# Optimization experiments

Hardware: AMD Instinct MI355X
Metric: run time of the kernel (lower is better)

Reference implementation:

```python
import jax, jax.numpy as jnp
import numpy as np

NX = NY = 2048
DT = 0.01
DX = 1.0
DY = 1.0
RE = 1.0
NLEVEL = int(np.log2(NY)) + 1  # 12 levels


def pad_zero(x):
    # Dirichlet (zero) halo of width 1: matches boundary_condition_u/v/k/cw
    return jnp.pad(x, ((0, 0), (0, 0), (1, 1), (1, 1)))


def pad_edge(x):
    # Edge-replicate halo (incl. corners): matches boundary_condition_p
    return jnp.pad(x, ((0, 0), (0, 0), (1, 1), (1, 1)), mode='edge')


def conv2d(x, w, stride=1):
    return jax.lax.conv_general_dilated(
        x, w, (stride, stride), 'VALID',
        dimension_numbers=('NCHW', 'OIHW', 'NCHW'))


def upsample2(x):
    return jnp.repeat(jnp.repeat(x, 2, axis=2), 2, axis=3)


def pg_vector(u, v, pad_u, pad_v, k1, ADx_u, ADy_u, ADx_v, ADy_v, AD2_u, AD2_v, w_diff):
    # Petrov-Galerkin dissipation. pad_u/pad_v are the padded ORIGINAL velocities:
    # the torch code references the global values_uu/values_vv buffers here.
    k_u = 0.25 * DX * jnp.abs(0.5 * DX ** -3 * (jnp.abs(u) * DX + jnp.abs(v) * DY) * AD2_u) \
        / (0.001 + (jnp.abs(ADx_u) * DX ** -3 + jnp.abs(ADy_u) * DX ** -3) / 2.0)
    k_v = 0.25 * DY * jnp.abs(0.5 * DX ** -3 * (jnp.abs(u) * DX + jnp.abs(v) * DY) * AD2_v) \
        / (0.001 + (jnp.abs(ADx_v) * DX ** -3 + jnp.abs(ADy_v) * DX ** -3) / 2.0)
    k_u = jnp.minimum(k_u, k1)
    k_v = jnp.minimum(k_v, k1)
    k_uu = pad_zero(k_u)
    k_vv = pad_zero(k_v)
    k_x = 1.5 * (k_u * AD2_u + conv2d(pad_u * k_uu, w_diff) - u * conv2d(k_uu, w_diff))
    k_y = 1.5 * (k_v * AD2_v + conv2d(pad_v * k_vv, w_diff) - v * conv2d(k_vv, w_diff))
    return k_x, k_y


def f_cycle_mg(pad_u, pad_v, values_p, iteration, w_A, w_res, w_xadv, w_yadv):
    diag = w_A[0, 0, 1, 1]
    b = -(conv2d(pad_u, w_xadv) + conv2d(pad_v, w_yadv)) / DT
    w = jnp.zeros((1, 1, 2, 2), values_p.dtype)
    r = b
    for _ in range(iteration):
        w = jnp.zeros((1, 1, 2, 2), values_p.dtype)
        r = conv2d(pad_edge(values_p), w_A) - b
        r_s = [r]
        for _i in range(1, NLEVEL - 1):
            r = conv2d(r, w_res, stride=2)  # restriction down to 2x2
            r_s.append(r)
        for i in reversed(range(1, NLEVEL - 1)):
            w = w - conv2d(pad_zero(w), w_A) / diag + r_s[i] / diag  # Jacobi smooth
            w = upsample2(w)  # prolongation
        values_p = values_p - w
        values_p = values_p - conv2d(pad_edge(values_p), w_A) / diag + b / diag
    return values_p, w, r


def setup_inputs() -> dict:
    key = jax.random.key(0)
    ku, kv, kp = jax.random.split(key, 3)
    shp = (1, 1, NY, NX)
    f32 = jnp.float32
    values_u = jax.random.normal(ku, shp, f32) * 0.1
    values_v = jax.random.normal(kv, shp, f32) * 0.1
    values_p = jax.random.normal(kp, shp, f32) * 0.1
    Fx = jnp.zeros(shp, f32)
    Fy = jnp.zeros(shp, f32)
    k1 = jnp.ones(shp, f32) * (DX ** 2 / DT)
    # FD stencils (learned conv params in the torch module)
    w_xadv = jnp.array([[0., 0., 0.], [-0.5, 0., 0.5], [0., 0., 0.]], f32).reshape(1, 1, 3, 3) / DX
    w_yadv = jnp.array([[0., -0.5, 0.], [0., 0., 0.], [0., 0.5, 0.]], f32).reshape(1, 1, 3, 3) / DY
    lap = jnp.array([[0., 1., 0.], [1., -4., 1.], [0., 1., 0.]], f32).reshape(1, 1, 3, 3) / DX ** 2
    w_diff = lap
    w_A = lap  # diag = -4
    w_res = jnp.full((1, 1, 2, 2), 0.25, f32)
    return dict(values_u=values_u, values_v=values_v, values_p=values_p,
                Fx=Fx, Fy=Fy, k1=k1,
                w_xadv=w_xadv, w_yadv=w_yadv, w_diff=w_diff, w_A=w_A, w_res=w_res,
                iteration=5)


def reference(values_u, values_v, values_p, Fx, Fy, k1,
              w_xadv, w_yadv, w_diff, w_A, w_res, iteration):
    pad_u = pad_zero(values_u)
    pad_v = pad_zero(values_v)
    pad_p = pad_edge(values_p)
    Grapx_p = conv2d(pad_p, w_xadv) * DT
    Grapy_p = conv2d(pad_p, w_yadv) * DT
    ADx_u = conv2d(pad_u, w_xadv); ADy_u = conv2d(pad_u, w_yadv)
    ADx_v = conv2d(pad_v, w_xadv); ADy_v = conv2d(pad_v, w_yadv)
    AD2_u = conv2d(pad_u, w_diff); AD2_v = conv2d(pad_v, w_diff)
    k_x, k_y = pg_vector(values_u, values_v, pad_u, pad_v, k1,
                         ADx_u, ADy_u, ADx_v, ADy_v, AD2_u, AD2_v, w_diff)
    b_u = values_u + 0.5 * (RE * k_x * DT - values_u * ADx_u * DT - values_v * ADy_u * DT) - Grapx_p - Fx * DT * 0
    b_v = values_v + 0.5 * (RE * k_y * DT - values_u * ADx_v * DT - values_v * ADy_v * DT) - Grapy_p - Fy * DT * 0
    pad_bu = pad_zero(b_u)
    pad_bv = pad_zero(b_v)
    ADx_u = conv2d(pad_bu, w_xadv); ADy_u = conv2d(pad_bu, w_yadv)
    ADx_v = conv2d(pad_bv, w_xadv); ADy_v = conv2d(pad_bv, w_yadv)
    AD2_u = conv2d(pad_bu, w_diff); AD2_v = conv2d(pad_bv, w_diff)
    # torch code closes over the global padded ORIGINAL velocities here (pad_u, pad_v)
    k_x, k_y = pg_vector(b_u, b_v, pad_u, pad_v, k1,
                         ADx_u, ADy_u, ADx_v, ADy_v, AD2_u, AD2_v, w_diff)
    values_u = values_u + RE * k_x * DT - b_u * ADx_u * DT - b_v * ADy_u * DT - Grapx_p - Fx * DT
    values_v = values_v + RE * k_y * DT - b_u * ADx_v * DT - b_v * ADy_v * DT - Grapy_p - Fy * DT
    values_p, w, r = f_cycle_mg(pad_zero(values_u), pad_zero(values_v), values_p,
                                iteration, w_A, w_res, w_xadv, w_yadv)
    pad_p2 = pad_edge(values_p)
    values_u = values_u - conv2d(pad_p2, w_xadv) * DT
    values_v = values_v - conv2d(pad_p2, w_yadv) * DT
    return values_u, values_v, values_p, w, r
```

## Files before the change

kernel.cpp:

```cpp
#include <hip/hip_runtime.h>

#define NN 2048
#define NN2 (NN * NN)

__device__ __forceinline__ void load6z(const float* __restrict__ A, int i, int j0, float a[6]) {
    if ((unsigned)i >= (unsigned)NN) {
#pragma unroll
        for (int q = 0; q < 6; ++q) a[q] = 0.f;
        return;
    }
    const float* row = A + (size_t)i * NN;
    float4 c = *reinterpret_cast<const float4*>(row + j0);
    a[1] = c.x; a[2] = c.y; a[3] = c.z; a[4] = c.w;
    a[0] = (j0 > 0) ? row[j0 - 1] : 0.f;
    a[5] = (j0 + 4 < NN) ? row[j0 + 4] : 0.f;
}
__device__ __forceinline__ void load4z(const float* __restrict__ A, int i, int j0, float a[4]) {
    if ((unsigned)i >= (unsigned)NN) {
#pragma unroll
        for (int q = 0; q < 4; ++q) a[q] = 0.f;
        return;
    }
    float4 c = *reinterpret_cast<const float4*>(A + (size_t)i * NN + j0);
    a[0] = c.x; a[1] = c.y; a[2] = c.z; a[3] = c.w;
}
__device__ __forceinline__ void load6e(const float* __restrict__ A, int i, int j0, float a[6]) {
    i = i < 0 ? 0 : (i > NN - 1 ? NN - 1 : i);
    const float* row = A + (size_t)i * NN;
    float4 c = *reinterpret_cast<const float4*>(row + j0);
    a[1] = c.x; a[2] = c.y; a[3] = c.z; a[4] = c.w;
    a[0] = (j0 > 0) ? row[j0 - 1] : c.x;
    a[5] = (j0 + 4 < NN) ? row[j0 + 4] : c.w;
}
__device__ __forceinline__ void load4e(const float* __restrict__ A, int i, int j0, float a[4]) {
    i = i < 0 ? 0 : (i > NN - 1 ? NN - 1 : i);
    float4 c = *reinterpret_cast<const float4*>(A + (size_t)i * NN + j0);
    a[0] = c.x; a[1] = c.y; a[2] = c.z; a[3] = c.w;
}
__device__ __forceinline__ void store4(float* __restrict__ A, int i, int j0, const float a[4]) {
    *reinterpret_cast<float4*>(A + (size_t)i * NN + j0) = make_float4(a[0], a[1], a[2], a[3]);
}

__global__ __launch_bounds__(256) void k_pred_f(const float* __restrict__ u, const float* __restrict__ v,
                                                const float* __restrict__ k1, const float* __restrict__ p,
                                                float* __restrict__ bu, float* __restrict__ bv) {
    const float DT = 0.01f;
    __shared__ __align__(16) float su[36][72], sv[36][72];
    __shared__ float sku[34][68], skv[34][68];
    const int jb = blockIdx.x * 64;
    const int ib = blockIdx.y * 32;
    const int tid = threadIdx.y * 16 + threadIdx.x;

    for (int idx = tid; idx < 36 * 18; idx += 256) {
        int r = idx / 18, c4 = idx - r * 18;
        int gi = ib - 2 + r;
        int gj = jb - 4 + c4 * 4;
        float4 uu = make_float4(0.f, 0.f, 0.f, 0.f), vv = uu;
        if ((unsigned)gi < (unsigned)NN) {
            if (gj >= 0 && gj + 3 < NN) {
                uu = *reinterpret_cast<const float4*>(u + (size_t)gi * NN + gj);
                vv = *reinterpret_cast<const float4*>(v + (size_t)gi * NN + gj);
            } else {
                float tu[4], tv[4];
#pragma unroll
                for (int q = 0; q < 4; ++q) {
                    int g = gj + q;
                    bool in = (unsigned)g < (unsigned)NN;
                    tu[q] = in ? u[(size_t)gi * NN + g] : 0.f;
                    tv[q] = in ? v[(size_t)gi * NN + g] : 0.f;
                }
                uu = make_float4(tu[0], tu[1], tu[2], tu[3]);
                vv = make_float4(tv[0], tv[1], tv[2], tv[3]);
            }
        }
        *reinterpret_cast<float4*>(&su[r][c4 * 4]) = uu;
        *reinterpret_cast<float4*>(&sv[r][c4 * 4]) = vv;
    }
    __syncthreads();

    for (int idx = tid; idx < 34 * 66; idx += 256) {
        int r = idx / 66, c = idx - r * 66;
        int gi = ib - 1 + r, gj = jb - 1 + c;
        float kuo = 0.f, kvo = 0.f;
        if ((unsigned)gi < (unsigned)NN && (unsigned)gj < (unsigned)NN) {
            int lr = r + 1, lc = c + 3;
            float uc = su[lr][lc], ul = su[lr][lc - 1], ur = su[lr][lc + 1], ut = su[lr - 1][lc], ub = su[lr + 1][lc];
            float vc = sv[lr][lc], vl = sv[lr][lc - 1], vr = sv[lr][lc + 1], vt = sv[lr - 1][lc], vb = sv[lr + 1][lc];
            float ADxu = 0.5f * (ur - ul), ADyu = 0.5f * (ub - ut);
            float ADxv = 0.5f * (vr - vl), ADyv = 0.5f * (vb - vt);
            float Lu = ul + ur + ut + ub - 4.f * uc;
            float Lv = vl + vr + vt + vb - 4.f * vc;
            float s = fabsf(uc) + fabsf(vc);
            float kuv = 0.25f * fabsf(0.5f * s * Lu) / (0.001f + 0.5f * (fabsf(ADxu) + fabsf(ADyu)));
            float kvv = 0.25f * fabsf(0.5f * s * Lv) / (0.001f + 0.5f * (fabsf(ADxv) + fabsf(ADyv)));
            float k1c = k1[(size_t)gi * NN + gj];
            kuo = fminf(kuv, k1c);
            kvo = fminf(kvv, k1c);
        }
        sku[r][c] = kuo;
        skv[r][c] = kvo;
    }
    __syncthreads();

    const int i0 = ib + threadIdx.y * 2;
    const int j0 = jb + threadIdx.x * 4;
#pragma unroll
    for (int a = 0; a < 2; ++a) {
        int i = i0 + a;
        float p6[6], pu[4], pd[4], obu[4], obv[4];
        load6e(p, i, j0, p6); load4e(p, i - 1, j0, pu); load4e(p, i + 1, j0, pd);
        int lur = i - ib + 2, lkr = i - ib + 1;
#pragma unroll
        for (int c = 0; c < 4; ++c) {
            int luc = j0 + c - jb + 4, lkc = j0 + c - jb + 1;
            float uc = su[lur][luc], ul = su[lur][luc - 1], ur = su[lur][luc + 1], ut = su[lur - 1][luc], ub = su[lur + 1][luc];
            float vc = sv[lur][luc], vl = sv[lur][luc - 1], vr = sv[lur][luc + 1], vt = sv[lur - 1][luc], vb = sv[lur + 1][luc];
            float kuc = sku[lkr][lkc], kul = sku[lkr][lkc - 1], kur = sku[lkr][lkc + 1], kut = sku[lkr - 1][lkc], kub = sku[lkr + 1][lkc];
            float kvc = skv[lkr][lkc], kvl = skv[lkr][lkc - 1], kvr = skv[lkr][lkc + 1], kvt = skv[lkr - 1][lkc], kvb = skv[lkr + 1][lkc];
            float ADxu = 0.5f * (ur - ul), ADyu = 0.5f * (ub - ut);
            float ADxv = 0.5f * (vr - vl), ADyv = 0.5f * (vb - vt);
            float Lu = ul + ur + ut + ub - 4.f * uc;
            float Lv = vl + vr + vt + vb - 4.f * vc;
            float Lku = kul + kur + kut + kub - 4.f * kuc;
            float Lkv = kvl + kvr + kvt + kvb - 4.f * kvc;
            float Luku = ul * kul + ur * kur + ut * kut + ub * kub - 4.f * uc * kuc;
            float Lvkv = vl * kvl + vr * kvr + vt * kvt + vb * kvb - 4.f * vc * kvc;
            float kx = 1.5f * (kuc * Lu + Luku - uc * Lku);
            float ky = 1.5f * (kvc * Lv + Lvkv - vc * Lkv);
            float Grapx = 0.5f * (p6[c + 2] - p6[c]) * DT;
            float Grapy = 0.5f * (pd[c] - pu[c]) * DT;
            obu[c] = uc + 0.5f * (kx * DT - uc * ADxu * DT - vc * ADyu * DT) - Grapx;
            obv[c] = vc + 0.5f * (ky * DT - uc * ADxv * DT - vc * ADyv * DT) - Grapy;
        }
        store4(bu, i, j0, obu);
        store4(bv, i, j0, obv);
    }
}

__global__ __launch_bounds__(256) void k_corr_f(const float* __restrict__ u, const float* __restrict__ v,
                                                const float* __restrict__ k1, const float* __restrict__ p,
                                                const float* __restrict__ bu, const float* __restrict__ bv,
                                                const float* __restrict__ Fx, const float* __restrict__ Fy,
                                                float* __restrict__ un, float* __restrict__ vn) {
    const float DT = 0.01f;
    __shared__ __align__(16) float sbu[36][72], sbv[36][72];
    __shared__ float sku[34][68], skv[34][68];
    const int jb = blockIdx.x * 64;
    const int ib = blockIdx.y * 32;
    const int tid = threadIdx.y * 16 + threadIdx.x;

    for (int idx = tid; idx < 36 * 18; idx += 256) {
        int r = idx / 18, c4 = idx - r * 18;
        int gi = ib - 2 + r;
        int gj = jb - 4 + c4 * 4;
        float4 uu = make_float4(0.f, 0.f, 0.f, 0.f), vv = uu;
        if ((unsigned)gi < (unsigned)NN) {
            if (gj >= 0 && gj + 3 < NN) {
                uu = *reinterpret_cast<const float4*>(bu + (size_t)gi * NN + gj);
                vv = *reinterpret_cast<const float4*>(bv + (size_t)gi * NN + gj);
            } else {
                float tu[4], tv[4];
#pragma unroll
                for (int q = 0; q < 4; ++q) {
                    int g = gj + q;
                    bool in = (unsigned)g < (unsigned)NN;
                    tu[q] = in ? bu[(size_t)gi * NN + g] : 0.f;
                    tv[q] = in ? bv[(size_t)gi * NN + g] : 0.f;
                }
                uu = make_float4(tu[0], tu[1], tu[2], tu[3]);
                vv = make_float4(tv[0], tv[1], tv[2], tv[3]);
            }
        }
        *reinterpret_cast<float4*>(&sbu[r][c4 * 4]) = uu;
        *reinterpret_cast<float4*>(&sbv[r][c4 * 4]) = vv;
    }
    __syncthreads();

    for (int idx = tid; idx < 34 * 66; idx += 256) {
        int r = idx / 66, c = idx - r * 66;
        int gi = ib - 1 + r, gj = jb - 1 + c;
        float kuo = 0.f, kvo = 0.f;
        if ((unsigned)gi < (unsigned)NN && (unsigned)gj < (unsigned)NN) {
            int lr = r + 1, lc = c + 3;
            float uc = sbu[lr][lc], ul = sbu[lr][lc - 1], ur = sbu[lr][lc + 1], ut = sbu[lr - 1][lc], ub = sbu[lr + 1][lc];
            float vc = sbv[lr][lc], vl = sbv[lr][lc - 1], vr = sbv[lr][lc + 1], vt = sbv[lr - 1][lc], vb = sbv[lr + 1][lc];
            float ADxu = 0.5f * (ur - ul), ADyu = 0.5f * (ub - ut);
            float ADxv = 0.5f * (vr - vl), ADyv = 0.5f * (vb - vt);
            float Lu = ul + ur + ut + ub - 4.f * uc;
            float Lv = vl + vr + vt + vb - 4.f * vc;
            float s = fabsf(uc) + fabsf(vc);
            float kuv = 0.25f * fabsf(0.5f * s * Lu) / (0.001f + 0.5f * (fabsf(ADxu) + fabsf(ADyu)));
            float kvv = 0.25f * fabsf(0.5f * s * Lv) / (0.001f + 0.5f * (fabsf(ADxv) + fabsf(ADyv)));
            float k1c = k1[(size_t)gi * NN + gj];
            kuo = fminf(kuv, k1c);
            kvo = fminf(kvv, k1c);
        }
        sku[r][c] = kuo;
        skv[r][c] = kvo;
    }
    __syncthreads();

    const int i0 = ib + threadIdx.y * 2;
    const int j0 = jb + threadIdx.x * 4;
#pragma unroll
    for (int a = 0; a < 2; ++a) {
        int i = i0 + a;
        float p6[6], pu[4], pd[4];
        float u6[6], uu[4], ud[4], v6[6], vu[4], vd[4], fx[4], fy[4], oun[4], ovn[4];
        load6e(p, i, j0, p6); load4e(p, i - 1, j0, pu); load4e(p, i + 1, j0, pd);
        load6z(u, i, j0, u6); load4z(u, i - 1, j0, uu); load4z(u, i + 1, j0, ud);
        load6z(v, i, j0, v6); load4z(v, i - 1, j0, vu); load4z(v, i + 1, j0, vd);
        load4z(Fx, i, j0, fx); load4z(Fy, i, j0, fy);
        int lbr = i - ib + 2, lkr = i - ib + 1;
#pragma unroll
        for (int c = 0; c < 4; ++c) {
            int lbc = j0 + c - jb + 4, lkc = j0 + c - jb + 1;
            float buc = sbu[lbr][lbc], bul = sbu[lbr][lbc - 1], bur = sbu[lbr][lbc + 1], but = sbu[lbr - 1][lbc], bub = sbu[lbr + 1][lbc];
            float bvc = sbv[lbr][lbc], bvl = sbv[lbr][lbc - 1], bvr = sbv[lbr][lbc + 1], bvt = sbv[lbr - 1][lbc], bvb = sbv[lbr + 1][lbc];
            float kuc = sku[lkr][lkc], kul = sku[lkr][lkc - 1], kur = sku[lkr][lkc + 1], kut = sku[lkr - 1][lkc], kub = sku[lkr + 1][lkc];
            float kvc = skv[lkr][lkc], kvl = skv[lkr][lkc - 1], kvr = skv[lkr][lkc + 1], kvt = skv[lkr - 1][lkc], kvb = skv[lkr + 1][lkc];
            float uc = u6[c + 1], ul = u6[c], ur = u6[c + 2], ut = uu[c], ub = ud[c];
            float vc = v6[c + 1], vl = v6[c], vr = v6[c + 2], vt = vu[c], vb = vd[c];
            float ADxbu = 0.5f * (bur - bul), ADybu = 0.5f * (bub - but);
            float ADxbv = 0.5f * (bvr - bvl), ADybv = 0.5f * (bvb - bvt);
            float Lbu = bul + bur + but + bub - 4.f * buc;
            float Lbv = bvl + bvr + bvt + bvb - 4.f * bvc;
            float Lku = kul + kur + kut + kub - 4.f * kuc;
            float Lkv = kvl + kvr + kvt + kvb - 4.f * kvc;
            float Luku = ul * kul + ur * kur + ut * kut + ub * kub - 4.f * uc * kuc;
            float Lvkv = vl * kvl + vr * kvr + vt * kvt + vb * kvb - 4.f * vc * kvc;
            float kx = 1.5f * (kuc * Lbu + Luku - buc * Lku);
            float ky = 1.5f * (kvc * Lbv + Lvkv - bvc * Lkv);
            float Grapx = 0.5f * (p6[c + 2] - p6[c]) * DT;
            float Grapy = 0.5f * (pd[c] - pu[c]) * DT;
            oun[c] = uc + kx * DT - buc * ADxbu * DT - bvc * ADybu * DT - Grapx - fx[c] * DT;
            ovn[c] = vc + ky * DT - buc * ADxbv * DT - bvc * ADybv * DT - Grapy - fy[c] * DT;
        }
        store4(un, i, j0, oun);
        store4(vn, i, j0, ovn);
    }
}

__global__ __launch_bounds__(256) void k_rhs_res(const float* __restrict__ un, const float* __restrict__ vn,
                                                 const float* __restrict__ p, float* __restrict__ b,
                                                 float* __restrict__ r1024, float* __restrict__ r512,
                                                 float* __restrict__ r256, float* __restrict__ r128) {
    __shared__ float s512r[4][64];
    __shared__ float s256r[2][32];
    int tx = threadIdx.x, ty = threadIdx.y;
    int jt = blockIdx.x * 64 + tx;
    int it = blockIdx.y * 4 + ty;
    int j0 = jt * 4, i0 = it * 4;
    float bb[4][4];
#pragma unroll
    for (int r = 0; r < 4; ++r) {
        float u6[6], vu[4], vd[4];
        load6z(un, i0 + r, j0, u6);
        load4z(vn, i0 + r - 1, j0, vu);
        load4z(vn, i0 + r + 1, j0, vd);
#pragma unroll
        for (int c = 0; c < 4; ++c)
            bb[r][c] = -100.f * (0.5f * (u6[c + 2] - u6[c]) + 0.5f * (vd[c] - vu[c]));
        store4(b, i0 + r, j0, bb[r]);
    }
    float p6[6][6];
#pragma unroll
    for (int r = 0; r < 6; ++r) load6e(p, i0 - 1 + r, j0, p6[r]);
    float res[4][4];
#pragma unroll
    for (int r = 0; r < 4; ++r)
#pragma unroll
        for (int c = 0; c < 4; ++c) {
            float pc = p6[r + 1][c + 1];
            res[r][c] = p6[r][c + 1] + p6[r + 2][c + 1] + p6[r + 1][c] + p6[r + 1][c + 2] - 4.f * pc - bb[r][c];
        }
    float q00 = 0.25f * (res[0][0] + res[0][1] + res[1][0] + res[1][1]);
    float q01 = 0.25f * (res[0][2] + res[0][3] + res[1][2] + res[1][3]);
    float q10 = 0.25f * (res[2][0] + res[2][1] + res[3][0] + res[3][1]);
    float q11 = 0.25f * (res[2][2] + res[2][3] + res[3][2] + res[3][3]);
    int ci = it * 2, cj = jt * 2;
    *reinterpret_cast<float2*>(r1024 + (size_t)ci * 1024 + cj)       = make_float2(q00, q01);
    *reinterpret_cast<float2*>(r1024 + (size_t)(ci + 1) * 1024 + cj) = make_float2(q10, q11);
    float s = 0.25f * (q00 + q01 + q10 + q11);
    r512[(size_t)it * 512 + jt] = s;
    s512r[ty][tx] = s;
    __syncthreads();
    int tid = ty * 64 + tx;
    if (tid < 64) {
        int a = tid >> 5, c = tid & 31;
        float m = 0.25f * (s512r[2 * a][2 * c] + s512r[2 * a][2 * c + 1] + s512r[2 * a + 1][2 * c] + s512r[2 * a + 1][2 * c + 1]);
        r256[(size_t)(blockIdx.y * 2 + a) * 256 + blockIdx.x * 32 + c] = m;
        s256r[a][c] = m;
    }
    __syncthreads();
    if (tid < 16) {
        float m = 0.25f * (s256r[0][2 * tid] + s256r[0][2 * tid + 1] + s256r[1][2 * tid] + s256r[1][2 * tid + 1]);
        r128[(size_t)blockIdx.y * 128 + blockIdx.x * 16 + tid] = m;
    }
}

__global__ __launch_bounds__(1024) void k_small(const float* __restrict__ r128,
                                                float* __restrict__ w128_out,
                                                float* __restrict__ r2_out) {
    __shared__ float sr64[64 * 64];
    __shared__ float sr32[32 * 32];
    __shared__ float sr16[16 * 16];
    __shared__ float sr8[8 * 8];
    __shared__ float sr4[16];
    __shared__ float sr2[4];
    __shared__ float wa[64 * 64];
    __shared__ float wb[64 * 64];
    int t = threadIdx.x;

    for (int idx = t; idx < 64 * 64; idx += 1024) {
        int i = idx >> 6, j = idx & 63;
        const float* s0 = r128 + (2 * i) * 128 + 2 * j;
        sr64[idx] = 0.25f * (s0[0] + s0[1] + s0[128] + s0[129]);
    }
    __syncthreads();
    if (t < 32 * 32) {
        int i = t >> 5, j = t & 31;
        const float* s0 = sr64 + (2 * i) * 64 + 2 * j;
        sr32[t] = 0.25f * (s0[0] + s0[1] + s0[64] + s0[65]);
    }
    __syncthreads();
    if (t < 16 * 16) {
        int i = t >> 4, j = t & 15;
        const float* s0 = sr32 + (2 * i) * 32 + 2 * j;
        sr16[t] = 0.25f * (s0[0] + s0[1] + s0[32] + s0[33]);
    }
    __syncthreads();
    if (t < 64) {
        int i = t >> 3, j = t & 7;
        const float* s0 = sr16 + (2 * i) * 16 + 2 * j;
        sr8[t] = 0.25f * (s0[0] + s0[1] + s0[16] + s0[17]);
    }
    __syncthreads();
    if (t < 16) {
        int i = t >> 2, j = t & 3;
        const float* s0 = sr8 + (2 * i) * 8 + 2 * j;
        sr4[t] = 0.25f * (s0[0] + s0[1] + s0[8] + s0[9]);
    }
    __syncthreads();
    if (t < 4) {
        int i = t >> 1, j = t & 1;
        const float* s0 = sr4 + (2 * i) * 4 + 2 * j;
        sr2[t] = 0.25f * (s0[0] + s0[1] + s0[4] + s0[5]);
        r2_out[t] = sr2[t];
        float ws = -0.25f * sr2[t];
        wa[(2 * i) * 4 + 2 * j] = ws;
        wa[(2 * i) * 4 + 2 * j + 1] = ws;
        wa[(2 * i + 1) * 4 + 2 * j] = ws;
        wa[(2 * i + 1) * 4 + 2 * j + 1] = ws;
    }
    __syncthreads();

    auto step = [&](const float* win, const float* rl, float* wout, int s) {
        for (int idx = t; idx < s * s; idx += 1024) {
            int i = idx / s, j = idx - i * s;
            float up = i > 0 ? win[(i - 1) * s + j] : 0.f;
            float dn = i < s - 1 ? win[(i + 1) * s + j] : 0.f;
            float lf = j > 0 ? win[i * s + j - 1] : 0.f;
            float rt = j < s - 1 ? win[i * s + j + 1] : 0.f;
            float ws = 0.25f * (up + dn + lf + rt - rl[idx]);
            int o = 2 * s;
            wout[(2 * i) * o + 2 * j] = ws;
            wout[(2 * i) * o + 2 * j + 1] = ws;
            wout[(2 * i + 1) * o + 2 * j] = ws;
            wout[(2 * i + 1) * o + 2 * j + 1] = ws;
        }
    };
    step(wa, sr4, wb, 4);
    __syncthreads();
    step(wb, sr8, wa, 8);
    __syncthreads();
    step(wa, sr16, wb, 16);
    __syncthreads();
    step(wb, sr32, wa, 32);
    __syncthreads();
    step(wa, sr64, w128_out, 64);
}

template <bool LAST>
__global__ __launch_bounds__(256) void k_mg_step(
    const float* __restrict__ p, const float* __restrict__ b,
    const float* __restrict__ w128,
    const float* __restrict__ r128, const float* __restrict__ r256,
    const float* __restrict__ r512, const float* __restrict__ r1024,
    float* __restrict__ pdst,
    float* __restrict__ o1024, float* __restrict__ o512,
    float* __restrict__ o256, float* __restrict__ o128,
    float* __restrict__ wout, float* __restrict__ un, float* __restrict__ vn)
{
    __shared__ float sw128[5][20];
    __shared__ float s128[3][18];
    __shared__ float s256[4][34];
    __shared__ float s512[6][66];
    __shared__ float s1024[10][132];
    __shared__ __align__(16) float pmid[20][264];
    __shared__ float pnew[18][258];
    __shared__ float red512[4][64];
    __shared__ float red256[2][32];

    const int jb = blockIdx.x * 256;
    const int ib = blockIdx.y * 16;
    const int tid = threadIdx.y * 64 + threadIdx.x;
    const int r1 = ib / 2 - 1,  c1 = jb / 2 - 1;
    const int r2 = ib / 4 - 1,  c2 = jb / 4 - 1;
    const int r3 = ib / 8 - 1,  c3 = jb / 8 - 1;
    const int r4 = ib / 16 - 1, c4 = jb / 16 - 1;
    const int r5 = ib / 16 - 2, c5 = jb / 16 - 2;

    if (tid < 100) {
        int r = tid / 20, c = tid - (tid / 20) * 20;
        int x = r5 + r, y = c5 + c;
        sw128[r][c] = ((unsigned)x < 128u && (unsigned)y < 128u) ? w128[x * 128 + y] : 0.f;
    }
    __syncthreads();
    if (tid < 54) {
        int r = tid / 18, c = tid - (tid / 18) * 18;
        int x = r4 + r, y = c4 + c;
        float v = 0.f;
        if ((unsigned)x < 128u && (unsigned)y < 128u) {
            float s = 0.f;
            if (x > 0)   s += sw128[r][c + 1];
            if (x < 127) s += sw128[r + 2][c + 1];
            if (y > 0)   s += sw128[r + 1][c];
            if (y < 127) s += sw128[r + 1][c + 2];
            v = 0.25f * (s - r128[x * 128 + y]);
        }
        s128[r][c] = v;
    }
    __syncthreads();
    if (tid < 136) {
        int r = tid / 34, c = tid - (tid / 34) * 34;
        int x = r3 + r, y = c3 + c;
        float v = 0.f;
        if ((unsigned)x < 256u && (unsigned)y < 256u) {
            float s = 0.f;
            if (x > 0)   s += s128[((x - 1) >> 1) - r4][(y >> 1) - c4];
            if (x < 255) s += s128[((x + 1) >> 1) - r4][(y >> 1) - c4];
            if (y > 0)   s += s128[(x >> 1) - r4][((y - 1) >> 1) - c4];
            if (y < 255) s += s128[(x >> 1) - r4][((y + 1) >> 1) - c4];
            v = 0.25f * (s - r256[x * 256 + y]);
        }
        s256[r][c] = v;
    }
    __syncthreads();
    for (int idx = tid; idx < 6 * 66; idx += 256) {
        int r = idx / 66, c = idx - (idx / 66) * 66;
        int x = r2 + r, y = c2 + c;
        float v = 0.f;
        if ((unsigned)x < 512u && (unsigned)y < 512u) {
            float s = 0.f;
            if (x > 0)   s += s256[((x - 1) >> 1) - r3][(y >> 1) - c3];
            if (x < 511) s += s256[((x + 1) >> 1) - r3][(y >> 1) - c3];
            if (y > 0)   s += s256[(x >> 1) - r3][((y - 1) >> 1) - c3];
            if (y < 511) s += s256[(x >> 1) - r3][((y + 1) >> 1) - c3];
            v = 0.25f * (s - r512[x * 512 + y]);
        }
        s512[r][c] = v;
    }
    __syncthreads();
    for (int idx = tid; idx < 10 * 130; idx += 256) {
        int r = idx / 130, c = idx - (idx / 130) * 130;
        int x = r1 + r, y = c1 + c;
        float v = 0.f;
        if ((unsigned)x < 1024u && (unsigned)y < 1024u) {
            float s = 0.f;
            if (x > 0)    s += s512[((x - 1) >> 1) - r2][(y >> 1) - c2];
            if (x < 1023) s += s512[((x + 1) >> 1) - r2][(y >> 1) - c2];
            if (y > 0)    s += s512[(x >> 1) - r2][((y - 1) >> 1) - c2];
            if (y < 1023) s += s512[(x >> 1) - r2][((y + 1) >> 1) - c2];
            v = 0.25f * (s - r1024[x * 1024 + y]);
        }
        s1024[r][c] = v;
    }
    __syncthreads();
    for (int idx = tid; idx < 20 * 66; idx += 256) {
        int r = idx / 66, q = idx - (idx / 66) * 66;
        int gi = ib - 2 + r;
        int gj0 = jb - 4 + q * 4;
        float vals[4] = {0.f, 0.f, 0.f, 0.f};
        if ((unsigned)gi < (unsigned)NN) {
            if (gj0 >= 0 && gj0 + 3 < NN) {
                float4 pv = *reinterpret_cast<const float4*>(p + (size_t)gi * NN + gj0);
                vals[0] = pv.x; vals[1] = pv.y; vals[2] = pv.z; vals[3] = pv.w;
            } else {
#pragma unroll
                for (int q4 = 0; q4 < 4; ++q4) {
                    int gj = gj0 + q4;
                    vals[q4] = ((unsigned)gj < (unsigned)NN) ? p[(size_t)gi * NN + gj] : 0.f;
                }
            }
        }
#pragma unroll
        for (int q4 = 0; q4 < 4; ++q4) {
            int gj = gj0 + q4;
            float m = 0.f;
            if ((unsigned)gi < (unsigned)NN && (unsigned)gj < (unsigned)NN &&
                gj >= jb - 2 && gj <= jb + 257) {
                m = vals[q4] - s1024[(gi >> 1) - r1][(gj >> 1) - c1];
            }
            pmid[r][q * 4 + q4] = m;
        }
    }
    __syncthreads();
    for (int idx = tid; idx < 18 * 258; idx += 256) {
        int r = idx / 258, c = idx - (idx / 258) * 258;
        int gi = ib - 1 + r, gj = jb - 1 + c;
        float v = 0.f;
        if ((unsigned)gi < (unsigned)NN && (unsigned)gj < (unsigned)NN) {
            int iu = gi > 0 ? gi - 1 : 0;
            int idn = gi < NN - 1 ? gi + 1 : NN - 1;
            int jl = gj > 0 ? gj - 1 : 0;
            int jr = gj < NN - 1 ? gj + 1 : NN - 1;
            float s = pmid[iu - (ib - 2)][gj - (jb - 4)] + pmid[idn - (ib - 2)][gj - (jb - 4)]
                    + pmid[gi - (ib - 2)][jl - (jb - 4)] + pmid[gi - (ib - 2)][jr - (jb - 4)];
            v = 0.25f * (s - b[(size_t)gi * NN + gj]);
        }
        pnew[r][c] = v;
    }
    __syncthreads();

    const int i0 = ib + threadIdx.y * 4;
    const int j0 = jb + threadIdx.x * 4;
#pragma unroll
    for (int rr = 0; rr < 4; ++rr) {
        int i = i0 + rr;
        int lr = i - (ib - 1);
        int lc = j0 - (jb - 1);
        *reinterpret_cast<float4*>(pdst + (size_t)i * NN + j0) =
            make_float4(pnew[lr][lc], pnew[lr][lc + 1], pnew[lr][lc + 2], pnew[lr][lc + 3]);
    }

    if (LAST) {
        const float DT = 0.01f;
#pragma unroll
        for (int rr = 0; rr < 4; ++rr) {
            int i = i0 + rr;
            int lr = i - (ib - 1);
            int s1r = (i >> 1) - r1;
            float ow[4];
#pragma unroll
            for (int c = 0; c < 4; ++c) ow[c] = s1024[s1r][((j0 + c) >> 1) - c1];
            store4(wout, i, j0, ow);
            float4 uu = *reinterpret_cast<float4*>(un + (size_t)i * NN + j0);
            float4 vv = *reinterpret_cast<float4*>(vn + (size_t)i * NN + j0);
            float ou[4] = {uu.x, uu.y, uu.z, uu.w};
            float ov[4] = {vv.x, vv.y, vv.z, vv.w};
            int iu = (i > 0 ? i - 1 : 0) - (ib - 1);
            int idn = (i < NN - 1 ? i + 1 : NN - 1) - (ib - 1);
#pragma unroll
            for (int c = 0; c < 4; ++c) {
                int j = j0 + c;
                int jl = (j > 0 ? j - 1 : 0) - (jb - 1);
                int jr = (j < NN - 1 ? j + 1 : NN - 1) - (jb - 1);
                int lc = j - (jb - 1);
                ou[c] -= 0.5f * (pnew[lr][jr] - pnew[lr][jl]) * DT;
                ov[c] -= 0.5f * (pnew[idn][lc] - pnew[iu][lc]) * DT;
            }
            store4(un, i, j0, ou);
            store4(vn, i, j0, ov);
        }
    } else {
        float res[4][4];
#pragma unroll
        for (int rr = 0; rr < 4; ++rr) {
#pragma unroll
            for (int cc = 0; cc < 4; ++cc) {
                int i = i0 + rr, j = j0 + cc;
                int lr = i - (ib - 1), lc = j - (jb - 1);
                int iu = (i > 0 ? i - 1 : 0) - (ib - 1);
                int idn = (i < NN - 1 ? i + 1 : NN - 1) - (ib - 1);
                int jl = (j > 0 ? j - 1 : 0) - (jb - 1);
                int jr = (j < NN - 1 ? j + 1 : NN - 1) - (jb - 1);
                res[rr][cc] = pnew[iu][lc] + pnew[idn][lc] + pnew[lr][jl] + pnew[lr][jr]
                            - 4.f * pnew[lr][lc] - b[(size_t)i * NN + j];
            }
        }
        int it = blockIdx.y * 4 + threadIdx.y;
        int jt = blockIdx.x * 64 + threadIdx.x;
        float q00 = 0.25f * (res[0][0] + res[0][1] + res[1][0] + res[1][1]);
        float q01 = 0.25f * (res[0][2] + res[0][3] + res[1][2] + res[1][3]);
        float q10 = 0.25f * (res[2][0] + res[2][1] + res[3][0] + res[3][1]);
        float q11 = 0.25f * (res[2][2] + res[2][3] + res[3][2] + res[3][3]);
        int ci = it * 2, cj = jt * 2;
        *reinterpret_cast<float2*>(o1024 + (size_t)ci * 1024 + cj)       = make_float2(q00, q01);
        *reinterpret_cast<float2*>(o1024 + (size_t)(ci + 1) * 1024 + cj) = make_float2(q10, q11);
        float s = 0.25f * (q00 + q01 + q10 + q11);
        o512[(size_t)it * 512 + jt] = s;
        red512[threadIdx.y][threadIdx.x] = s;
        __syncthreads();
        if (tid < 64) {
            int a = tid >> 5, c = tid & 31;
            float m = 0.25f * (red512[2 * a][2 * c] + red512[2 * a][2 * c + 1] +
                               red512[2 * a + 1][2 * c] + red512[2 * a + 1][2 * c + 1]);
            o256[(size_t)(blockIdx.y * 2 + a) * 256 + blockIdx.x * 32 + c] = m;
            red256[a][c] = m;
        }
        __syncthreads();
        if (tid < 16) {
            float m = 0.25f * (red256[0][2 * tid] + red256[0][2 * tid + 1] +
                               red256[1][2 * tid] + red256[1][2 * tid + 1]);
            o128[(size_t)blockIdx.y * 128 + blockIdx.x * 16 + tid] = m;
        }
    }
}

extern "C" void kernel_launch(void* const* d_in, const int* in_sizes, int n_in,
                              void* d_out, int out_size, void* d_ws, size_t ws_size,
                              hipStream_t stream) {
    const float* u  = (const float*)d_in[0];
    const float* v  = (const float*)d_in[1];
    const float* p  = (const float*)d_in[2];
    const float* Fx = (const float*)d_in[3];
    const float* Fy = (const float*)d_in[4];
    const float* k1 = (const float*)d_in[5];

    float* out = (float*)d_out;
    float* out_u = out;
    float* out_v = out + (size_t)NN2;
    float* out_p = out + 2 * (size_t)NN2;
    float* out_w = out + 3 * (size_t)NN2;
    float* out_r = out + 4 * (size_t)NN2;

    float* ws = (float*)d_ws;
    float* b  = ws;
    float* pA = ws + (size_t)NN2;
    float* pB = ws + 2 * (size_t)NN2;
    float* base = ws + 3 * (size_t)NN2;
    float* rA1024 = base;
    float* rA512  = rA1024 + 1024 * 1024;
    float* rA256  = rA512 + 512 * 512;
    float* rA128  = rA256 + 256 * 256;
    float* rB1024 = rA128 + 128 * 128;
    float* rB512  = rB1024 + 1024 * 1024;
    float* rB256  = rB512 + 512 * 512;
    float* rB128  = rB256 + 256 * 256;
    float* w128   = rB128 + 128 * 128;

    float* bu = out_w;
    float* bv = out_p;

    dim3 blk(64, 4);
    dim3 blkT(16, 16);
    dim3 gT(32, 64);
    dim3 gM(8, 128);

    k_pred_f<<<gT, blkT, 0, stream>>>(u, v, k1, p, bu, bv);
    k_corr_f<<<gT, blkT, 0, stream>>>(u, v, k1, p, bu, bv, Fx, Fy, out_u, out_v);
    k_rhs_res<<<gM, blk, 0, stream>>>(out_u, out_v, p, b, rA1024, rA512, rA256, rA128);

    const float* pcur = p;
    for (int it = 0; it < 5; ++it) {
        const bool useA = (it % 2 == 0);
        const float* R1024 = useA ? rA1024 : rB1024;
        const float* R512  = useA ? rA512  : rB512;
        const float* R256  = useA ? rA256  : rB256;
        const float* R128  = useA ? rA128  : rB128;
        float* O1024 = useA ? rB1024 : rA1024;
        float* O512  = useA ? rB512  : rA512;
        float* O256  = useA ? rB256  : rA256;
        float* O128  = useA ? rB128  : rA128;

        k_small<<<1, 1024, 0, stream>>>(R128, w128, out_r);
        if (it < 4) {
            float* pdst = (it & 1) ? pB : pA;
            k_mg_step<false><<<gM, blk, 0, stream>>>(pcur, b, w128, R128, R256, R512, R1024,
                                                     pdst, O1024, O512, O256, O128,
                                                     nullptr, nullptr, nullptr);
            pcur = pdst;
        } else {
            k_mg_step<true><<<gM, blk, 0, stream>>>(pcur, b, w128, R128, R256, R512, R1024,
                                                    out_p, nullptr, nullptr, nullptr, nullptr,
                                                    out_w, out_u, out_v);
        }
    }
}
```

Measured before the change: 459.1 us.

## Split multigrid step into prolongation and smaller-tile pressure update kernels

Adds a separate prolongation kernel that computes the 256-level correction and writes a 512x512 correction grid. The pressure update kernel now runs on smaller tiles with more blocks, and the 128-level restriction moves into the single-block coarse kernel. The predictor and corrector kernels use 16-row tiles instead of 32, which doubles the block count and lowers shared memory use per block. The aim is more parallelism and occupancy in the per-iteration kernel, at the cost of one extra launch per iteration, an extra 512x512 buffer round trip through memory, and more halo recomputation.

```diff
diff --git a/kernel.cpp b/kernel.cpp
--- a/kernel.cpp
+++ b/kernel.cpp
@@ -45,13 +45,13 @@
                                                 const float* __restrict__ k1, const float* __restrict__ p,
                                                 float* __restrict__ bu, float* __restrict__ bv) {
     const float DT = 0.01f;
-    __shared__ __align__(16) float su[36][72], sv[36][72];
-    __shared__ float sku[34][68], skv[34][68];
+    __shared__ __align__(16) float su[20][72], sv[20][72];
+    __shared__ float sku[18][68], skv[18][68];
     const int jb = blockIdx.x * 64;
-    const int ib = blockIdx.y * 32;
+    const int ib = blockIdx.y * 16;
     const int tid = threadIdx.y * 16 + threadIdx.x;
 
-    for (int idx = tid; idx < 36 * 18; idx += 256) {
+    for (int idx = tid; idx < 20 * 18; idx += 256) {
         int r = idx / 18, c4 = idx - r * 18;
         int gi = ib - 2 + r;
         int gj = jb - 4 + c4 * 4;
@@ -78,7 +78,7 @@
     }
     __syncthreads();
 
-    for (int idx = tid; idx < 34 * 66; idx += 256) {
+    for (int idx = tid; idx < 18 * 66; idx += 256) {
         int r = idx / 66, c = idx - r * 66;
         int gi = ib - 1 + r, gj = jb - 1 + c;
         float kuo = 0.f, kvo = 0.f;
@@ -102,39 +102,35 @@
     }
     __syncthreads();
 
-    const int i0 = ib + threadIdx.y * 2;
+    const int i = ib + threadIdx.y;
     const int j0 = jb + threadIdx.x * 4;
-#pragma unroll
-    for (int a = 0; a < 2; ++a) {
-        int i = i0 + a;
-        float p6[6], pu[4], pd[4], obu[4], obv[4];
-        load6e(p, i, j0, p6); load4e(p, i - 1, j0, pu); load4e(p, i + 1, j0, pd);
-        int lur = i - ib + 2, lkr = i - ib + 1;
-#pragma unroll
-        for (int c = 0; c < 4; ++c) {
-            int luc = j0 + c - jb + 4, lkc = j0 + c - jb + 1;
-            float uc = su[lur][luc], ul = su[lur][luc - 1], ur = su[lur][luc + 1], ut = su[lur - 1][luc], ub = su[lur + 1][luc];
-            float vc = sv[lur][luc], vl = sv[lur][luc - 1], vr = sv[lur][luc + 1], vt = sv[lur - 1][luc], vb = sv[lur + 1][luc];
-            float kuc = sku[lkr][lkc], kul = sku[lkr][lkc - 1], kur = sku[lkr][lkc + 1], kut = sku[lkr - 1][lkc], kub = sku[lkr + 1][lkc];
-            float kvc = skv[lkr][lkc], kvl = skv[lkr][lkc - 1], kvr = skv[lkr][lkc + 1], kvt = skv[lkr - 1][lkc], kvb = skv[lkr + 1][lkc];
-            float ADxu = 0.5f * (ur - ul), ADyu = 0.5f * (ub - ut);
-            float ADxv = 0.5f * (vr - vl), ADyv = 0.5f * (vb - vt);
-            float Lu = ul + ur + ut + ub - 4.f * uc;
-            float Lv = vl + vr + vt + vb - 4.f * vc;
-            float Lku = kul + kur + kut + kub - 4.f * kuc;
-            float Lkv = kvl + kvr + kvt + kvb - 4.f * kvc;
-            float Luku = ul * kul + ur * kur + ut * kut + ub * kub - 4.f * uc * kuc;
-            float Lvkv = vl * kvl + vr * kvr + vt * kvt + vb * kvb - 4.f * vc * kvc;
-            float kx = 1.5f * (kuc * Lu + Luku - uc * Lku);
-            float ky = 1.5f * (kvc * Lv + Lvkv - vc * Lkv);
-            float Grapx = 0.5f * (p6[c + 2] - p6[c]) * DT;
-            float Grapy = 0.5f * (pd[c] - pu[c]) * DT;
-            obu[c] = uc + 0.5f * (kx * DT - uc * ADxu * DT - vc * ADyu * DT) - Grapx;
-            obv[c] = vc + 0.5f * (ky * DT - uc * ADxv * DT - vc * ADyv * DT) - Grapy;
-        }
-        store4(bu, i, j0, obu);
-        store4(bv, i, j0, obv);
-    }
+    float p6[6], pu[4], pd[4], obu[4], obv[4];
+    load6e(p, i, j0, p6); load4e(p, i - 1, j0, pu); load4e(p, i + 1, j0, pd);
+    const int lur = threadIdx.y + 2, lkr = threadIdx.y + 1;
+#pragma unroll
+    for (int c = 0; c < 4; ++c) {
+        int luc = threadIdx.x * 4 + c + 4, lkc = threadIdx.x * 4 + c + 1;
+        float uc = su[lur][luc], ul = su[lur][luc - 1], ur = su[lur][luc + 1], ut = su[lur - 1][luc], ub = su[lur + 1][luc];
+        float vc = sv[lur][luc], vl = sv[lur][luc - 1], vr = sv[lur][luc + 1], vt = sv[lur - 1][luc], vb = sv[lur + 1][luc];
+        float kuc = sku[lkr][lkc], kul = sku[lkr][lkc - 1], kur = sku[lkr][lkc + 1], kut = sku[lkr - 1][lkc], kub = sku[lkr + 1][lkc];
+        float kvc = skv[lkr][lkc], kvl = skv[lkr][lkc - 1], kvr = skv[lkr][lkc + 1], kvt = skv[lkr - 1][lkc], kvb = skv[lkr + 1][lkc];
+        float ADxu = 0.5f * (ur - ul), ADyu = 0.5f * (ub - ut);
+        float ADxv = 0.5f * (vr - vl), ADyv = 0.5f * (vb - vt);
+        float Lu = ul + ur + ut + ub - 4.f * uc;
+        float Lv = vl + vr + vt + vb - 4.f * vc;
+        float Lku = kul + kur + kut + kub - 4.f * kuc;
+        float Lkv = kvl + kvr + kvt + kvb - 4.f * kvc;
+        float Luku = ul * kul + ur * kur + ut * kut + ub * kub - 4.f * uc * kuc;
+        float Lvkv = vl * kvl + vr * kvr + vt * kvt + vb * kvb - 4.f * vc * kvc;
+        float kx = 1.5f * (kuc * Lu + Luku - uc * Lku);
+        float ky = 1.5f * (kvc * Lv + Lvkv - vc * Lkv);
+        float Grapx = 0.5f * (p6[c + 2] - p6[c]) * DT;
+        float Grapy = 0.5f * (pd[c] - pu[c]) * DT;
+        obu[c] = uc + 0.5f * (kx * DT - uc * ADxu * DT - vc * ADyu * DT) - Grapx;
+        obv[c] = vc + 0.5f * (ky * DT - uc * ADxv * DT - vc * ADyv * DT) - Grapy;
+    }
+    store4(bu, i, j0, obu);
+    store4(bv, i, j0, obv);
 }
 
 __global__ __launch_bounds__(256) void k_corr_f(const float* __restrict__ u, const float* __restrict__ v,
@@ -143,13 +139,13 @@
                                                 const float* __restrict__ Fx, const float* __restrict__ Fy,
                                                 float* __restrict__ un, float* __restrict__ vn) {
     const float DT = 0.01f;
-    __shared__ __align__(16) float sbu[36][72], sbv[36][72];
-    __shared__ float sku[34][68], skv[34][68];
+    __shared__ __align__(16) float sbu[20][72], sbv[20][72];
+    __shared__ float sku[18][68], skv[18][68];
     const int jb = blockIdx.x * 64;
-    const int ib = blockIdx.y * 32;
+    const int ib = blockIdx.y * 16;
     const int tid = threadIdx.y * 16 + threadIdx.x;
 
-    for (int idx = tid; idx < 36 * 18; idx += 256) {
+    for (int idx = tid; idx < 20 * 18; idx += 256) {
         int r = idx / 18, c4 = idx - r * 18;
         int gi = ib - 2 + r;
         int gj = jb - 4 + c4 * 4;
@@ -176,7 +172,7 @@
     }
     __syncthreads();
 
-    for (int idx = tid; idx < 34 * 66; idx += 256) {
+    for (int idx = tid; idx < 18 * 66; idx += 256) {
         int r = idx / 66, c = idx - r * 66;
         int gi = ib - 1 + r, gj = jb - 1 + c;
         float kuo = 0.f, kvo = 0.f;
@@ -200,53 +196,48 @@
     }
     __syncthreads();
 
-    const int i0 = ib + threadIdx.y * 2;
+    const int i = ib + threadIdx.y;
     const int j0 = jb + threadIdx.x * 4;
-#pragma unroll
-    for (int a = 0; a < 2; ++a) {
-        int i = i0 + a;
-        float p6[6], pu[4], pd[4];
-        float u6[6], uu[4], ud[4], v6[6], vu[4], vd[4], fx[4], fy[4], oun[4], ovn[4];
-        load6e(p, i, j0, p6); load4e(p, i - 1, j0, pu); load4e(p, i + 1, j0, pd);
-        load6z(u, i, j0, u6); load4z(u, i - 1, j0, uu); load4z(u, i + 1, j0, ud);
-        load6z(v, i, j0, v6); load4z(v, i - 1, j0, vu); load4z(v, i + 1, j0, vd);
-        load4z(Fx, i, j0, fx); load4z(Fy, i, j0, fy);
-        int lbr = i - ib + 2, lkr = i - ib + 1;
-#pragma unroll
-        for (int c = 0; c < 4; ++c) {
-            int lbc = j0 + c - jb + 4, lkc = j0 + c - jb + 1;
-            float buc = sbu[lbr][lbc], bul = sbu[lbr][lbc - 1], bur = sbu[lbr][lbc + 1], but = sbu[lbr - 1][lbc], bub = sbu[lbr + 1][lbc];
-            float bvc = sbv[lbr][lbc], bvl = sbv[lbr][lbc - 1], bvr = sbv[lbr][lbc + 1], bvt = sbv[lbr - 1][lbc], bvb = sbv[lbr + 1][lbc];
-            float kuc = sku[lkr][lkc], kul = sku[lkr][lkc - 1], kur = sku[lkr][lkc + 1], kut = sku[lkr - 1][lkc], kub = sku[lkr + 1][lkc];
-            float kvc = skv[lkr][lkc], kvl = skv[lkr][lkc - 1], kvr = skv[lkr][lkc + 1], kvt = skv[lkr - 1][lkc], kvb = skv[lkr + 1][lkc];
-            float uc = u6[c + 1], ul = u6[c], ur = u6[c + 2], ut = uu[c], ub = ud[c];
-            float vc = v6[c + 1], vl = v6[c], vr = v6[c + 2], vt = vu[c], vb = vd[c];
-            float ADxbu = 0.5f * (bur - bul), ADybu = 0.5f * (bub - but);
-            float ADxbv = 0.5f * (bvr - bvl), ADybv = 0.5f * (bvb - bvt);
-            float Lbu = bul + bur + but + bub - 4.f * buc;
-            float Lbv = bvl + bvr + bvt + bvb - 4.f * bvc;
-            float Lku = kul + kur + kut + kub - 4.f * kuc;
-            float Lkv = kvl + kvr + kvt + kvb - 4.f * kvc;
-            float Luku = ul * kul + ur * kur + ut * kut + ub * kub - 4.f * uc * kuc;
-            float Lvkv = vl * kvl + vr * kvr + vt * kvt + vb * kvb - 4.f * vc * kvc;
-            float kx = 1.5f * (kuc * Lbu + Luku - buc * Lku);
-            float ky = 1.5f * (kvc * Lbv + Lvkv - bvc * Lkv);
-            float Grapx = 0.5f * (p6[c + 2] - p6[c]) * DT;
-            float Grapy = 0.5f * (pd[c] - pu[c]) * DT;
-            oun[c] = uc + kx * DT - buc * ADxbu * DT - bvc * ADybu * DT - Grapx - fx[c] * DT;
-            ovn[c] = vc + ky * DT - buc * ADxbv * DT - bvc * ADybv * DT - Grapy - fy[c] * DT;
-        }
-        store4(un, i, j0, oun);
-        store4(vn, i, j0, ovn);
-    }
+    float p6[6], pu[4], pd[4];
+    float u6[6], uu[4], ud[4], v6[6], vu[4], vd[4], fx[4], fy[4], oun[4], ovn[4];
+    load6e(p, i, j0, p6); load4e(p, i - 1, j0, pu); load4e(p, i + 1, j0, pd);
+    load6z(u, i, j0, u6); load4z(u, i - 1, j0, uu); load4z(u, i + 1, j0, ud);
+    load6z(v, i, j0, v6); load4z(v, i - 1, j0, vu); load4z(v, i + 1, j0, vd);
+    load4z(Fx, i, j0, fx); load4z(Fy, i, j0, fy);
+    const int lbr = threadIdx.y + 2, lkr = threadIdx.y + 1;
+#pragma unroll
+    for (int c = 0; c < 4; ++c) {
+        int lbc = threadIdx.x * 4 + c + 4, lkc = threadIdx.x * 4 + c + 1;
+        float buc = sbu[lbr][lbc], bul = sbu[lbr][lbc - 1], bur = sbu[lbr][lbc + 1], but = sbu[lbr - 1][lbc], bub = sbu[lbr + 1][lbc];
+        float bvc = sbv[lbr][lbc], bvl = sbv[lbr][lbc - 1], bvr = sbv[lbr][lbc + 1], bvt = sbv[lbr - 1][lbc], bvb = sbv[lbr + 1][lbc];
+        float kuc = sku[lkr][lkc], kul = sku[lkr][lkc - 1], kur = sku[lkr][lkc + 1], kut = sku[lkr - 1][lkc], kub = sku[lkr + 1][lkc];
+        float kvc = skv[lkr][lkc], kvl = skv[lkr][lkc - 1], kvr = skv[lkr][lkc + 1], kvt = skv[lkr - 1][lkc], kvb = skv[lkr + 1][lkc];
+        float uc = u6[c + 1], ul = u6[c], ur = u6[c + 2], ut = uu[c], ub = ud[c];
+        float vc = v6[c + 1], vl = v6[c], vr = v6[c + 2], vt = vu[c], vb = vd[c];
+        float ADxbu = 0.5f * (bur - bul), ADybu = 0.5f * (bub - but);
+        float ADxbv = 0.5f * (bvr - bvl), ADybv = 0.5f * (bvb - bvt);
+        float Lbu = bul + bur + but + bub - 4.f * buc;
+        float Lbv = bvl + bvr + bvt + bvb - 4.f * bvc;
+        float Lku = kul + kur + kut + kub - 4.f * kuc;
+        float Lkv = kvl + kvr + kvt + kvb - 4.f * kvc;
+        float Luku = ul * kul + ur * kur + ut * kut + ub * kub - 4.f * uc * kuc;
+        float Lvkv = vl * kvl + vr * kvr + vt * kvt + vb * kvb - 4.f * vc * kvc;
+        float kx = 1.5f * (kuc * Lbu + Luku - buc * Lku);
+        float ky = 1.5f * (kvc * Lbv + Lvkv - bvc * Lkv);
+        float Grapx = 0.5f * (p6[c + 2] - p6[c]) * DT;
+        float Grapy = 0.5f * (pd[c] - pu[c]) * DT;
+        oun[c] = uc + kx * DT - buc * ADxbu * DT - bvc * ADybu * DT - Grapx - fx[c] * DT;
+        ovn[c] = vc + ky * DT - buc * ADxbv * DT - bvc * ADybv * DT - Grapy - fy[c] * DT;
+    }
+    store4(un, i, j0, oun);
+    store4(vn, i, j0, ovn);
 }
 
 __global__ __launch_bounds__(256) void k_rhs_res(const float* __restrict__ un, const float* __restrict__ vn,
                                                  const float* __restrict__ p, float* __restrict__ b,
                                                  float* __restrict__ r1024, float* __restrict__ r512,
-                                                 float* __restrict__ r256, float* __restrict__ r128) {
+                                                 float* __restrict__ r256) {
     __shared__ float s512r[4][64];
-    __shared__ float s256r[2][32];
     int tx = threadIdx.x, ty = threadIdx.y;
     int jt = blockIdx.x * 64 + tx;
     int it = blockIdx.y * 4 + ty;
@@ -290,18 +281,14 @@
         int a = tid >> 5, c = tid & 31;
         float m = 0.25f * (s512r[2 * a][2 * c] + s512r[2 * a][2 * c + 1] + s512r[2 * a + 1][2 * c] + s512r[2 * a + 1][2 * c + 1]);
         r256[(size_t)(blockIdx.y * 2 + a) * 256 + blockIdx.x * 32 + c] = m;
-        s256r[a][c] = m;
-    }
-    __syncthreads();
-    if (tid < 16) {
-        float m = 0.25f * (s256r[0][2 * tid] + s256r[0][2 * tid + 1] + s256r[1][2 * tid] + s256r[1][2 * tid + 1]);
-        r128[(size_t)blockIdx.y * 128 + blockIdx.x * 16 + tid] = m;
-    }
-}
-
-__global__ __launch_bounds__(1024) void k_small(const float* __restrict__ r128,
-                                                float* __restrict__ w128_out,
-                                                float* __restrict__ r2_out) {
+    }
+}
+
+__global__ __launch_bounds__(1024) void k_small2(const float* __restrict__ r256in,
+                                                 float* __restrict__ r128g,
+                                                 float* __restrict__ w128_out,
+                                                 float* __restrict__ r2_out) {
+    __shared__ float sr128[128 * 128];
     __shared__ float sr64[64 * 64];
     __shared__ float sr32[32 * 32];
     __shared__ float sr16[16 * 16];
@@ -312,9 +299,17 @@
     __shared__ float wb[64 * 64];
     int t = threadIdx.x;
 
+    for (int idx = t; idx < 128 * 128; idx += 1024) {
+        int i = idx >> 7, j = idx & 127;
+        const float* s0 = r256in + (2 * i) * 256 + 2 * j;
+        float m = 0.25f * (s0[0] + s0[1] + s0[256] + s0[257]);
+        sr128[idx] = m;
+        r128g[idx] = m;
+    }
+    __syncthreads();
     for (int idx = t; idx < 64 * 64; idx += 1024) {
         int i = idx >> 6, j = idx & 63;
-        const float* s0 = r128 + (2 * i) * 128 + 2 * j;
+        const float* s0 = sr128 + (2 * i) * 128 + 2 * j;
         sr64[idx] = 0.25f * (s0[0] + s0[1] + s0[128] + s0[129]);
     }
     __syncthreads();
@@ -381,104 +376,114 @@
     step(wa, sr64, w128_out, 64);
 }
 
+__global__ __launch_bounds__(256) void k_prolong2(const float* __restrict__ w128, const float* __restrict__ r128,
+                                                  const float* __restrict__ r256, float* __restrict__ w512) {
+    __shared__ float sw[5][68];
+    __shared__ float s128[3][66];
+    __shared__ float s256[2][128];
+    const int jb = blockIdx.x * 256;
+    const int ob = blockIdx.y * 4;
+    const int by = blockIdx.y;
+    const int rw = by - 2, cw = jb / 4 - 2;
+    const int rs = by - 1, cs = jb / 4 - 1;
+    const int tid = threadIdx.y * 64 + threadIdx.x;
+
+    for (int idx = tid; idx < 5 * 68; idx += 256) {
+        int r = idx / 68, c = idx - r * 68;
+        int x = rw + r, y = cw + c;
+        sw[r][c] = ((unsigned)x < 128u && (unsigned)y < 128u) ? w128[x * 128 + y] : 0.f;
+    }
+    __syncthreads();
+    if (tid < 3 * 66) {
+        int r = tid / 66, c = tid - (tid / 66) * 66;
+        int x = rs + r, y = cs + c;
+        float val = 0.f;
+        if ((unsigned)x < 128u && (unsigned)y < 128u) {
+            int lr = r + 1, lc = c + 1;
+            val = 0.25f * (sw[lr - 1][lc] + sw[lr + 1][lc] + sw[lr][lc - 1] + sw[lr][lc + 1] - r128[x * 128 + y]);
+        }
+        s128[r][c] = val;
+    }
+    __syncthreads();
+    {
+        int rr = tid >> 7, cc = tid & 127;
+        int X = 2 * by + rr, Y = jb / 2 + cc;
+        float s = 0.f;
+        if (X > 0)   s += s128[((X - 1) >> 1) - rs][(Y >> 1) - cs];
+        if (X < 255) s += s128[((X + 1) >> 1) - rs][(Y >> 1) - cs];
+        if (Y > 0)   s += s128[(X >> 1) - rs][((Y - 1) >> 1) - cs];
+        if (Y < 255) s += s128[(X >> 1) - rs][((Y + 1) >> 1) - cs];
+        s256[rr][cc] = 0.25f * (s - r256[X * 256 + Y]);
+    }
+    __syncthreads();
+    const int i = ob + threadIdx.y;
+    const int j0 = jb + threadIdx.x * 4;
+    const int lr = (i >> 1) - 2 * by;
+    float o[4];
+#pragma unroll
+    for (int c = 0; c < 4; ++c) o[c] = s256[lr][((j0 + c) >> 1) - jb / 2];
+    *reinterpret_cast<float4*>(w512 + (size_t)i * 512 + j0) = make_float4(o[0], o[1], o[2], o[3]);
+}
+
 template <bool LAST>
-__global__ __launch_bounds__(256) void k_mg_step(
+__global__ __launch_bounds__(256) void k_pupd3(
     const float* __restrict__ p, const float* __restrict__ b,
-    const float* __restrict__ w128,
-    const float* __restrict__ r128, const float* __restrict__ r256,
-    const float* __restrict__ r512, const float* __restrict__ r1024,
+    const float* __restrict__ w512, const float* __restrict__ r512,
+    const float* __restrict__ r1024,
     float* __restrict__ pdst,
-    float* __restrict__ o1024, float* __restrict__ o512,
-    float* __restrict__ o256, float* __restrict__ o128,
+    float* __restrict__ o1024, float* __restrict__ o512, float* __restrict__ o256,
     float* __restrict__ wout, float* __restrict__ un, float* __restrict__ vn)
 {
-    __shared__ float sw128[5][20];
-    __shared__ float s128[3][18];
-    __shared__ float s256[4][34];
-    __shared__ float s512[6][66];
-    __shared__ float s1024[10][132];
-    __shared__ __align__(16) float pmid[20][264];
-    __shared__ float pnew[18][258];
-    __shared__ float red512[4][64];
-    __shared__ float red256[2][32];
-
-    const int jb = blockIdx.x * 256;
-    const int ib = blockIdx.y * 16;
-    const int tid = threadIdx.y * 64 + threadIdx.x;
-    const int r1 = ib / 2 - 1,  c1 = jb / 2 - 1;
-    const int r2 = ib / 4 - 1,  c2 = jb / 4 - 1;
-    const int r3 = ib / 8 - 1,  c3 = jb / 8 - 1;
-    const int r4 = ib / 16 - 1, c4 = jb / 16 - 1;
-    const int r5 = ib / 16 - 2, c5 = jb / 16 - 2;
-
-    if (tid < 100) {
-        int r = tid / 20, c = tid - (tid / 20) * 20;
-        int x = r5 + r, y = c5 + c;
-        sw128[r][c] = ((unsigned)x < 128u && (unsigned)y < 128u) ? w128[x * 128 + y] : 0.f;
-    }
-    __syncthreads();
-    if (tid < 54) {
-        int r = tid / 18, c = tid - (tid / 18) * 18;
-        int x = r4 + r, y = c4 + c;
-        float v = 0.f;
-        if ((unsigned)x < 128u && (unsigned)y < 128u) {
-            float s = 0.f;
-            if (x > 0)   s += sw128[r][c + 1];
-            if (x < 127) s += sw128[r + 2][c + 1];
-            if (y > 0)   s += sw128[r + 1][c];
-            if (y < 127) s += sw128[r + 1][c + 2];
-            v = 0.25f * (s - r128[x * 128 + y]);
-        }
-        s128[r][c] = v;
-    }
-    __syncthreads();
-    if (tid < 136) {
-        int r = tid / 34, c = tid - (tid / 34) * 34;
+    __shared__ float sW[6][38];
+    __shared__ float sS[4][36];
+    __shared__ float ws[6][68];
+    __shared__ __align__(16) float pmid[12][136];
+    __shared__ float pnew[10][130];
+    __shared__ float sq[4][64];
+    __shared__ float red[2][32];
+
+    const int jb = blockIdx.x * 128;
+    const int ib = blockIdx.y * 8;
+    const int tid = threadIdx.y * 32 + threadIdx.x;
+    const int r1 = ib / 2 - 1, c1 = jb / 2 - 2;
+    const int r2 = ib / 4 - 1, c2 = jb / 4 - 2;
+    const int r3 = ib / 4 - 2, c3 = jb / 4 - 3;
+
+    for (int idx = tid; idx < 6 * 38; idx += 256) {
+        int r = idx / 38, c = idx - r * 38;
         int x = r3 + r, y = c3 + c;
-        float v = 0.f;
-        if ((unsigned)x < 256u && (unsigned)y < 256u) {
-            float s = 0.f;
-            if (x > 0)   s += s128[((x - 1) >> 1) - r4][(y >> 1) - c4];
-            if (x < 255) s += s128[((x + 1) >> 1) - r4][(y >> 1) - c4];
-            if (y > 0)   s += s128[(x >> 1) - r4][((y - 1) >> 1) - c4];
-            if (y < 255) s += s128[(x >> 1) - r4][((y + 1) >> 1) - c4];
-            v = 0.25f * (s - r256[x * 256 + y]);
-        }
-        s256[r][c] = v;
-    }
-    __syncthreads();
-    for (int idx = tid; idx < 6 * 66; idx += 256) {
-        int r = idx / 66, c = idx - (idx / 66) * 66;
+        sW[r][c] = ((unsigned)x < 512u && (unsigned)y < 512u) ? w512[(size_t)x * 512 + y] : 0.f;
+    }
+    __syncthreads();
+    if (tid < 4 * 36) {
+        int r = tid / 36, c = tid - (tid / 36) * 36;
         int x = r2 + r, y = c2 + c;
-        float v = 0.f;
+        float val = 0.f;
         if ((unsigned)x < 512u && (unsigned)y < 512u) {
-            float s = 0.f;
-            if (x > 0)   s += s256[((x - 1) >> 1) - r3][(y >> 1) - c3];
-            if (x < 511) s += s256[((x + 1) >> 1) - r3][(y >> 1) - c3];
-            if (y > 0)   s += s256[(x >> 1) - r3][((y - 1) >> 1) - c3];
-            if (y < 511) s += s256[(x >> 1) - r3][((y + 1) >> 1) - c3];
-            v = 0.25f * (s - r512[x * 512 + y]);
-        }
-        s512[r][c] = v;
-    }
-    __syncthreads();
-    for (int idx = tid; idx < 10 * 130; idx += 256) {
-        int r = idx / 130, c = idx - (idx / 130) * 130;
+            int lr = r + 1, lc = c + 1;
+            val = 0.25f * (sW[lr - 1][lc] + sW[lr + 1][lc] + sW[lr][lc - 1] + sW[lr][lc + 1]
+                           - r512[(size_t)x * 512 + y]);
+        }
+        sS[r][c] = val;
+    }
+    __syncthreads();
+    for (int idx = tid; idx < 6 * 68; idx += 256) {
+        int r = idx / 68, c = idx - r * 68;
         int x = r1 + r, y = c1 + c;
-        float v = 0.f;
+        float val = 0.f;
         if ((unsigned)x < 1024u && (unsigned)y < 1024u) {
             float s = 0.f;
-            if (x > 0)    s += s512[((x - 1) >> 1) - r2][(y >> 1) - c2];
-            if (x < 1023) s += s512[((x + 1) >> 1) - r2][(y >> 1) - c2];
-            if (y > 0)    s += s512[(x >> 1) - r2][((y - 1) >> 1) - c2];
-            if (y < 1023) s += s512[(x >> 1) - r2][((y + 1) >> 1) - c2];
-            v = 0.25f * (s - r1024[x * 1024 + y]);
-        }
-        s1024[r][c] = v;
-    }
-    __syncthreads();
-    for (int idx = tid; idx < 20 * 66; idx += 256) {
-        int r = idx / 66, q = idx - (idx / 66) * 66;
+            if (x > 0)    s += sS[((x - 1) >> 1) - r2][(y >> 1) - c2];
+            if (x < 1023) s += sS[((x + 1) >> 1) - r2][(y >> 1) - c2];
+            if (y > 0)    s += sS[(x >> 1) - r2][((y - 1) >> 1) - c2];
+            if (y < 1023) s += sS[(x >> 1) - r2][((y + 1) >> 1) - c2];
+            val = 0.25f * (s - r1024[(size_t)x * 1024 + y]);
+        }
+        ws[r][c] = val;
+    }
+    __syncthreads();
+    for (int idx = tid; idx < 12 * 34; idx += 256) {
+        int r = idx / 34, q = idx - r * 34;
         int gi = ib - 2 + r;
         int gj0 = jb - 4 + q * 4;
         float vals[4] = {0.f, 0.f, 0.f, 0.f};
@@ -499,17 +504,17 @@
             int gj = gj0 + q4;
             float m = 0.f;
             if ((unsigned)gi < (unsigned)NN && (unsigned)gj < (unsigned)NN &&
-                gj >= jb - 2 && gj <= jb + 257) {
-                m = vals[q4] - s1024[(gi >> 1) - r1][(gj >> 1) - c1];
+                gj >= jb - 2 && gj <= jb + 129) {
+                m = vals[q4] - ws[(gi >> 1) - r1][(gj >> 1) - c1];
             }
             pmid[r][q * 4 + q4] = m;
         }
     }
     __syncthreads();
-    for (int idx = tid; idx < 18 * 258; idx += 256) {
-        int r = idx / 258, c = idx - (idx / 258) * 258;
+    for (int idx = tid; idx < 10 * 130; idx += 256) {
+        int r = idx / 130, c = idx - r * 130;
         int gi = ib - 1 + r, gj = jb - 1 + c;
-        float v = 0.f;
+        float val = 0.f;
         if ((unsigned)gi < (unsigned)NN && (unsigned)gj < (unsigned)NN) {
             int iu = gi > 0 ? gi - 1 : 0;
             int idn = gi < NN - 1 ? gi + 1 : NN - 1;
@@ -517,93 +522,76 @@
             int jr = gj < NN - 1 ? gj + 1 : NN - 1;
             float s = pmid[iu - (ib - 2)][gj - (jb - 4)] + pmid[idn - (ib - 2)][gj - (jb - 4)]
                     + pmid[gi - (ib - 2)][jl - (jb - 4)] + pmid[gi - (ib - 2)][jr - (jb - 4)];
-            v = 0.25f * (s - b[(size_t)gi * NN + gj]);
-        }
-        pnew[r][c] = v;
-    }
-    __syncthreads();
-
-    const int i0 = ib + threadIdx.y * 4;
+            val = 0.25f * (s - b[(size_t)gi * NN + gj]);
+        }
+        pnew[r][c] = val;
+    }
+    __syncthreads();
+
+    const int i  = ib + threadIdx.y;
     const int j0 = jb + threadIdx.x * 4;
-#pragma unroll
-    for (int rr = 0; rr < 4; ++rr) {
-        int i = i0 + rr;
-        int lr = i - (ib - 1);
-        int lc = j0 - (jb - 1);
-        *reinterpret_cast<float4*>(pdst + (size_t)i * NN + j0) =
-            make_float4(pnew[lr][lc], pnew[lr][lc + 1], pnew[lr][lc + 2], pnew[lr][lc + 3]);
-    }
+    const int lr = i - (ib - 1);
+    const int lc = j0 - (jb - 1);
+    *reinterpret_cast<float4*>(pdst + (size_t)i * NN + j0) =
+        make_float4(pnew[lr][lc], pnew[lr][lc + 1], pnew[lr][lc + 2], pnew[lr][lc + 3]);
 
     if (LAST) {
         const float DT = 0.01f;
-#pragma unroll
-        for (int rr = 0; rr < 4; ++rr) {
-            int i = i0 + rr;
-            int lr = i - (ib - 1);
-            int s1r = (i >> 1) - r1;
-            float ow[4];
-#pragma unroll
-            for (int c = 0; c < 4; ++c) ow[c] = s1024[s1r][((j0 + c) >> 1) - c1];
-            store4(wout, i, j0, ow);
-            float4 uu = *reinterpret_cast<float4*>(un + (size_t)i * NN + j0);
-            float4 vv = *reinterpret_cast<float4*>(vn + (size_t)i * NN + j0);
-            float ou[4] = {uu.x, uu.y, uu.z, uu.w};
-            float ov[4] = {vv.x, vv.y, vv.z, vv.w};
-            int iu = (i > 0 ? i - 1 : 0) - (ib - 1);
-            int idn = (i < NN - 1 ? i + 1 : NN - 1) - (ib - 1);
-#pragma unroll
-            for (int c = 0; c < 4; ++c) {
-                int j = j0 + c;
-                int jl = (j > 0 ? j - 1 : 0) - (jb - 1);
-                int jr = (j < NN - 1 ? j + 1 : NN - 1) - (jb - 1);
-                int lc = j - (jb - 1);
-                ou[c] -= 0.5f * (pnew[lr][jr] - pnew[lr][jl]) * DT;
-                ov[c] -= 0.5f * (pnew[idn][lc] - pnew[iu][lc]) * DT;
+        float ow[4];
+        int wr = (i >> 1) - r1;
+#pragma unroll
+        for (int c = 0; c < 4; ++c) ow[c] = ws[wr][((j0 + c) >> 1) - c1];
+        store4(wout, i, j0, ow);
+        float4 uu = *reinterpret_cast<float4*>(un + (size_t)i * NN + j0);
+        float4 vv = *reinterpret_cast<float4*>(vn + (size_t)i * NN + j0);
+        float ou[4] = {uu.x, uu.y, uu.z, uu.w};
+        float ov[4] = {vv.x, vv.y, vv.z, vv.w};
+        int iu = (i > 0 ? i - 1 : 0) - (ib - 1);
+        int idn = (i < NN - 1 ? i + 1 : NN - 1) - (ib - 1);
+#pragma unroll
+        for (int c = 0; c < 4; ++c) {
+            int j = j0 + c;
+            int jl = (j > 0 ? j - 1 : 0) - (jb - 1);
+            int jr = (j < NN - 1 ? j + 1 : NN - 1) - (jb - 1);
+            int lcc = j - (jb - 1);
+            ou[c] -= 0.5f * (pnew[lr][jr] - pnew[lr][jl]) * DT;
+            ov[c] -= 0.5f * (pnew[idn][lcc] - pnew[iu][lcc]) * DT;
+        }
+        store4(un, i, j0, ou);
+        store4(vn, i, j0, ov);
+    } else {
+        int cr = tid >> 6, cc = tid & 63;
+        float q = 0.f;
+#pragma unroll
+        for (int dr = 0; dr < 2; ++dr) {
+#pragma unroll
+            for (int dc = 0; dc < 2; ++dc) {
+                int i2 = ib + 2 * cr + dr, j2 = jb + 2 * cc + dc;
+                int lr2 = i2 - (ib - 1), lc2 = j2 - (jb - 1);
+                int iu2 = (i2 > 0 ? i2 - 1 : 0) - (ib - 1);
+                int id2 = (i2 < NN - 1 ? i2 + 1 : NN - 1) - (ib - 1);
+                int jl2 = (j2 > 0 ? j2 - 1 : 0) - (jb - 1);
+                int jr2 = (j2 < NN - 1 ? j2 + 1 : NN - 1) - (jb - 1);
+                q += pnew[iu2][lc2] + pnew[id2][lc2] + pnew[lr2][jl2] + pnew[lr2][jr2]
+                   - 4.f * pnew[lr2][lc2] - b[(size_t)i2 * NN + j2];
             }
-            store4(un, i, j0, ou);
-            store4(vn, i, j0, ov);
-        }
-    } else {
-        float res[4][4];
-#pragma unroll
-        for (int rr = 0; rr < 4; ++rr) {
-#pragma unroll
-            for (int cc = 0; cc < 4; ++cc) {
-                int i = i0 + rr, j = j0 + cc;
-                int lr = i - (ib - 1), lc = j - (jb - 1);
-                int iu = (i > 0 ? i - 1 : 0) - (ib - 1);
-                int idn = (i < NN - 1 ? i + 1 : NN - 1) - (ib - 1);
-                int jl = (j > 0 ? j - 1 : 0) - (jb - 1);
-                int jr = (j < NN - 1 ? j + 1 : NN - 1) - (jb - 1);
-                res[rr][cc] = pnew[iu][lc] + pnew[idn][lc] + pnew[lr][jl] + pnew[lr][jr]
-                            - 4.f * pnew[lr][lc] - b[(size_t)i * NN + j];
-            }
-        }
-        int it = blockIdx.y * 4 + threadIdx.y;
-        int jt = blockIdx.x * 64 + threadIdx.x;
-        float q00 = 0.25f * (res[0][0] + res[0][1] + res[1][0] + res[1][1]);
-        float q01 = 0.25f * (res[0][2] + res[0][3] + res[1][2] + res[1][3]);
-        float q10 = 0.25f * (res[2][0] + res[2][1] + res[3][0] + res[3][1]);
-        float q11 = 0.25f * (res[2][2] + res[2][3] + res[3][2] + res[3][3]);
-        int ci = it * 2, cj = jt * 2;
-        *reinterpret_cast<float2*>(o1024 + (size_t)ci * 1024 + cj)       = make_float2(q00, q01);
-        *reinterpret_cast<float2*>(o1024 + (size_t)(ci + 1) * 1024 + cj) = make_float2(q10, q11);
-        float s = 0.25f * (q00 + q01 + q10 + q11);
-        o512[(size_t)it * 512 + jt] = s;
-        red512[threadIdx.y][threadIdx.x] = s;
+        }
+        q *= 0.25f;
+        sq[cr][cc] = q;
+        o1024[(size_t)(ib / 2 + cr) * 1024 + jb / 2 + cc] = q;
         __syncthreads();
         if (tid < 64) {
-            int a = tid >> 5, c = tid & 31;
-            float m = 0.25f * (red512[2 * a][2 * c] + red512[2 * a][2 * c + 1] +
-                               red512[2 * a + 1][2 * c] + red512[2 * a + 1][2 * c + 1]);
-            o256[(size_t)(blockIdx.y * 2 + a) * 256 + blockIdx.x * 32 + c] = m;
-            red256[a][c] = m;
+            int rr = tid >> 5, c5 = tid & 31;
+            float m = 0.25f * (sq[2 * rr][2 * c5] + sq[2 * rr][2 * c5 + 1] +
+                               sq[2 * rr + 1][2 * c5] + sq[2 * rr + 1][2 * c5 + 1]);
+            o512[(size_t)(ib / 4 + rr) * 512 + jb / 4 + c5] = m;
+            red[rr][c5] = m;
         }
         __syncthreads();
         if (tid < 16) {
-            float m = 0.25f * (red256[0][2 * tid] + red256[0][2 * tid + 1] +
-                               red256[1][2 * tid] + red256[1][2 * tid + 1]);
-            o128[(size_t)blockIdx.y * 128 + blockIdx.x * 16 + tid] = m;
+            float m = 0.25f * (red[0][2 * tid] + red[0][2 * tid + 1] +
+                               red[1][2 * tid] + red[1][2 * tid + 1]);
+            o256[(size_t)(ib / 8) * 256 + jb / 8 + tid] = m;
         }
     }
 }
@@ -625,32 +613,35 @@
     float* out_w = out + 3 * (size_t)NN2;
     float* out_r = out + 4 * (size_t)NN2;
 
-    float* ws = (float*)d_ws;
-    float* b  = ws;
-    float* pA = ws + (size_t)NN2;
-    float* pB = ws + 2 * (size_t)NN2;
-    float* base = ws + 3 * (size_t)NN2;
+    float* wsb = (float*)d_ws;
+    float* b  = wsb;
+    float* pA = wsb + (size_t)NN2;
+    float* pB = wsb + 2 * (size_t)NN2;
+    float* base = wsb + 3 * (size_t)NN2;
     float* rA1024 = base;
     float* rA512  = rA1024 + 1024 * 1024;
     float* rA256  = rA512 + 512 * 512;
-    float* rA128  = rA256 + 256 * 256;
-    float* rB1024 = rA128 + 128 * 128;
+    float* rB1024 = rA256 + 256 * 256;
     float* rB512  = rB1024 + 1024 * 1024;
     float* rB256  = rB512 + 512 * 512;
-    float* rB128  = rB256 + 256 * 256;
-    float* w128   = rB128 + 128 * 128;
+    float* r128   = rB256 + 256 * 256;
+    float* w128   = r128 + 128 * 128;
+    float* w512   = w128 + 128 * 128;
 
     float* bu = out_w;
     float* bv = out_p;
 
-    dim3 blk(64, 4);
     dim3 blkT(16, 16);
-    dim3 gT(32, 64);
-    dim3 gM(8, 128);
+    dim3 gT(32, 128);
+    dim3 blkR(64, 4);
+    dim3 gR(8, 128);
+    dim3 blkP(32, 8);
+    dim3 gP(16, 256);
+    dim3 gL(2, 128);
 
     k_pred_f<<<gT, blkT, 0, stream>>>(u, v, k1, p, bu, bv);
     k_corr_f<<<gT, blkT, 0, stream>>>(u, v, k1, p, bu, bv, Fx, Fy, out_u, out_v);
-    k_rhs_res<<<gM, blk, 0, stream>>>(out_u, out_v, p, b, rA1024, rA512, rA256, rA128);
+    k_rhs_res<<<gR, blkR, 0, stream>>>(out_u, out_v, p, b, rA1024, rA512, rA256);
 
     const float* pcur = p;
     for (int it = 0; it < 5; ++it) {
@@ -658,23 +649,22 @@
         const float* R1024 = useA ? rA1024 : rB1024;
         const float* R512  = useA ? rA512  : rB512;
         const float* R256  = useA ? rA256  : rB256;
-        const float* R128  = useA ? rA128  : rB128;
         float* O1024 = useA ? rB1024 : rA1024;
         float* O512  = useA ? rB512  : rA512;
         float* O256  = useA ? rB256  : rA256;
-        float* O128  = useA ? rB128  : rA128;
-
-        k_small<<<1, 1024, 0, stream>>>(R128, w128, out_r);
+
+        k_small2<<<1, 1024, 0, stream>>>(R256, r128, w128, out_r);
+        k_prolong2<<<gL, blkR, 0, stream>>>(w128, r128, R256, w512);
         if (it < 4) {
             float* pdst = (it & 1) ? pB : pA;
-            k_mg_step<false><<<gM, blk, 0, stream>>>(pcur, b, w128, R128, R256, R512, R1024,
-                                                     pdst, O1024, O512, O256, O128,
-                                                     nullptr, nullptr, nullptr);
+            k_pupd3<false><<<gP, blkP, 0, stream>>>(pcur, b, w512, R512, R1024,
+                                                    pdst, O1024, O512, O256,
+                                                    nullptr, nullptr, nullptr);
             pcur = pdst;
         } else {
-            k_mg_step<true><<<gM, blk, 0, stream>>>(pcur, b, w128, R128, R256, R512, R1024,
-                                                    out_p, nullptr, nullptr, nullptr, nullptr,
-                                                    out_w, out_u, out_v);
-        }
-    }
-}
+            k_pupd3<true><<<gP, blkP, 0, stream>>>(pcur, b, w512, R512, R1024,
+                                                   out_p, nullptr, nullptr, nullptr,
+                                                   out_w, out_u, out_v);
+        }
+    }
+}
```

Measured after the change: 393.1 us. 14.4% less time.
